# Performance work log

Hardware: AMD Instinct MI355X
Metric: run time of the kernel (lower is better)

## Reference

```python
import jax, jax.numpy as jnp
import numpy as np
from jax import lax

B, V, M, C, CM, D = 48, 16, 32, 48, 8, 128
VOCAB_V, VOCAB_M, OUT = 2000, 1000, 256


def setup_inputs() -> dict:
    key = jax.random.key(0)
    ks = jax.random.split(key, 22)
    s = 0.1  # keep GRU gates out of saturation
    return {
        "visit_ids": jax.random.randint(ks[0], (3, B, V, C), 0, VOCAB_V),
        "mon_ids": jax.random.randint(ks[1], (4, B, V, M, CM), 0, VOCAB_M),
        "weight_vals": jax.random.uniform(ks[2], (B, V)),
        "age_vals": jax.random.uniform(ks[3], (B, V)),
        "emb_visit": jax.random.normal(ks[4], (3, VOCAB_V, D)) * s,
        "emb_mon": jax.random.normal(ks[5], (4, VOCAB_M, D)) * s,
        "mgru_Wih": jax.random.normal(ks[6], (5, 3 * D, D)) * s,
        "mgru_Whh": jax.random.normal(ks[7], (5, 3 * D, D)) * s,
        "mgru_bih": jax.random.normal(ks[8], (5, 3 * D)) * s,
        "mgru_bhh": jax.random.normal(ks[9], (5, 3 * D)) * s,
        "vgru_Wih": jax.random.normal(ks[10], (7, 3 * D, D)) * s,
        "vgru_Whh": jax.random.normal(ks[11], (7, 3 * D, D)) * s,
        "vgru_bih": jax.random.normal(ks[12], (7, 3 * D)) * s,
        "vgru_bhh": jax.random.normal(ks[13], (7, 3 * D)) * s,
        "fc_weight_w": jax.random.normal(ks[14], (D, 1)) * s,
        "fc_weight_b": jax.random.normal(ks[15], (D,)) * s,
        "fc_age_w": jax.random.normal(ks[16], (D, 1)) * s,
        "fc_age_b": jax.random.normal(ks[17], (D,)) * s,
        "fc_out_w": jax.random.normal(ks[18], (OUT, 7 * D)) * s,
        "fc_out_b": jax.random.normal(ks[19], (OUT,)) * s,
    }


def gru_last(x, Wih, Whh, bih, bhh):
    """torch.nn.GRU(batch_first=True), return final hidden [N, D]."""
    xi = jnp.einsum('ntd,ed->nte', x, Wih) + bih  # [N, T, 3D] input projections
    h0 = jnp.zeros((x.shape[0], Whh.shape[1]), x.dtype)

    def step(h, gi):
        gh = h @ Whh.T + bhh
        ir, iz, inn = jnp.split(gi, 3, axis=-1)
        hr, hz, hn = jnp.split(gh, 3, axis=-1)
        r = jax.nn.sigmoid(ir + hr)
        z = jax.nn.sigmoid(iz + hz)
        n = jnp.tanh(inn + r * hn)
        return (1.0 - z) * n + z * h, None

    hT, _ = lax.scan(step, h0, jnp.swapaxes(xi, 0, 1))
    return hT


def reference(visit_ids, mon_ids, weight_vals, age_vals, emb_visit, emb_mon,
              mgru_Wih, mgru_Whh, mgru_bih, mgru_bhh,
              vgru_Wih, vgru_Whh, vgru_bih, vgru_bhh,
              fc_weight_w, fc_weight_b, fc_age_w, fc_age_b,
              fc_out_w, fc_out_b):
    # padding_idx=0 -> zero embedding row (dropout in eval mode = identity)
    ev = emb_visit.at[:, 0].set(0.0)
    em = emb_mon.at[:, 0].set(0.0)

    # visit-event embedding-bag: sum over code dim -> [B, V, D] per feature
    visit_origin = [jnp.sum(ev[k][visit_ids[k]], axis=2) for k in range(3)]

    def run_stream(t, mi, vi):
        # monitor-level GRU over M, then visit-level GRU over V
        h1 = gru_last(t, mgru_Wih[mi], mgru_Whh[mi], mgru_bih[mi], mgru_bhh[mi])
        h2 = gru_last(h1.reshape(B, V, D),
                      vgru_Wih[vi], vgru_Whh[vi], vgru_bih[vi], vgru_bhh[vi])
        return h2  # [B, D]

    # output slots in dict-insertion order: lab_item, cond, proc, drug, inj_item, weight, age
    slots = [None] * 7
    for p in range(2):  # (lab_item, lab_value), (inj_item, inj_value)
        # elementwise item*value embedding, summed over codes -> [B*V, M, D]
        mon = jnp.sum(em[2 * p][mon_ids[2 * p]] * em[2 * p + 1][mon_ids[2 * p + 1]],
                      axis=3).reshape(B * V, M, D)
        slots[0 if p == 0 else 4] = run_stream(mon, p, p)
        for k in range(3):  # visit features repeated along monitor dim
            t = jnp.broadcast_to(visit_origin[k][:, :, None, :],
                                 (B, V, M, D)).reshape(B * V, M, D)
            h = run_stream(t, 2 + k, 2 + k)
            slots[1 + k] = h if slots[1 + k] is None else slots[1 + k] + h

    # weight / age: Linear(1->D), zero-mask, visit-level GRU
    for vals, w, b, vi, slot in ((weight_vals, fc_weight_w, fc_weight_b, 5, 5),
                                 (age_vals, fc_age_w, fc_age_b, 6, 6)):
        xf = vals.reshape(-1, 1)
        h = (xf @ w.T + b) * (xf != 0)
        slots[slot] = gru_last(h.reshape(B, V, D),
                               vgru_Wih[vi], vgru_Whh[vi], vgru_bih[vi], vgru_bhh[vi])

    patient_emb = jnp.concatenate(slots, axis=-1)  # [B, 7D]
    return jax.nn.relu(patient_emb) @ fc_out_w.T + fc_out_b
```

## Files before the change

kernel.cpp:

```cpp
#include <hip/hip_runtime.h>
#include <stdint.h>


typedef unsigned short u16;
typedef uint32_t u32;
typedef short bf8 __attribute__((ext_vector_type(8)));
typedef float f4 __attribute__((ext_vector_type(4)));

static __device__ __forceinline__ float bf2f(u16 b){ u32 u=((u32)b)<<16; float f; __builtin_memcpy(&f,&u,4); return f; }
static __device__ __forceinline__ u16 f2bf(float f){ u32 u; __builtin_memcpy(&u,&f,4); u32 r=(u+0x7fffu+((u>>16)&1u))>>16; return (u16)r; }
static __device__ __forceinline__ float bflo(u32 u){ u32 x=u<<16; float f; __builtin_memcpy(&f,&x,4); return f; }
static __device__ __forceinline__ float bfhi(u32 u){ u32 x=u&0xffff0000u; float f; __builtin_memcpy(&f,&x,4); return f; }
static __device__ __forceinline__ f4 mfma16(bf8 a, bf8 b, f4 c){ return __builtin_amdgcn_mfma_f32_16x16x32_bf16(a,b,c,0,0,0); }

#if __has_builtin(__builtin_amdgcn_exp2f)
static __device__ __forceinline__ float fexp2(float x){ return __builtin_amdgcn_exp2f(x); }
#else
static __device__ __forceinline__ float fexp2(float x){ float r; asm volatile("v_exp_f32 %0, %1" : "=v"(r) : "v"(x)); return r; }
#endif
#if __has_builtin(__builtin_amdgcn_rcpf)
static __device__ __forceinline__ float frcp(float x){ return __builtin_amdgcn_rcpf(x); }
#else
static __device__ __forceinline__ float frcp(float x){ float r; asm volatile("v_rcp_f32 %0, %1" : "=v"(r) : "v"(x)); return r; }
#endif
#define LOG2E 1.44269504089f
static __device__ __forceinline__ float sigm(float x){ return frcp(1.0f + fexp2(-LOG2E*x)); }
static __device__ __forceinline__ float tanh_f(float x){ return 1.0f - 2.0f*frcp(1.0f + fexp2((2.0f*LOG2E)*x)); }

__global__ __launch_bounds__(256) void k_prep(
    const float* __restrict__ s0, const float* __restrict__ s1,
    const float* __restrict__ s2, const float* __restrict__ s3,
    const float* __restrict__ s4, const float* __restrict__ s5,
    u16* __restrict__ d0, u16* __restrict__ d1, u16* __restrict__ d2,
    u16* __restrict__ d3, u16* __restrict__ d4, u16* __restrict__ d5){
  int i = blockIdx.x*256 + threadIdx.x;
  const float* s; u16* d; int off;
  if      (i < 61440)  { s=s0; d=d0; off=i; }
  else if (i < 122880) { s=s1; d=d1; off=i-61440; }
  else if (i < 208896) { s=s2; d=d2; off=i-122880; }
  else if (i < 294912) { s=s3; d=d3; off=i-208896; }
  else if (i < 422912) { s=s4; d=d4; off=i-294912; }
  else if (i < 614912) { s=s5; d=d5; off=i-422912; }
  else return;
  float4 v = *(const float4*)(s + (size_t)off*4);
  ushort4 o = { f2bf(v.x), f2bf(v.y), f2bf(v.z), f2bf(v.w) };
  *(ushort4*)(d + (size_t)off*4) = o;
}

__global__ __launch_bounds__(256) void k_bags(const int* __restrict__ vids, const int* __restrict__ mids,
    const u16* __restrict__ embv_b, const u16* __restrict__ embm_b,
    const float* __restrict__ wv, const float* __restrict__ av,
    const float* __restrict__ ww, const float* __restrict__ wb,
    const float* __restrict__ aw, const float* __restrict__ ab,
    u16* __restrict__ mon_xT, u16* __restrict__ vis_org, u16* __restrict__ hin2T){
  int y = blockIdx.y;
  if (y < 2){
    int p = y;
    int rid = threadIdx.x >> 5, lane32 = threadIdx.x & 31, d0 = lane32*4;
    __shared__ int ids[8][16];
    if (threadIdx.x < 128){
      int rr = threadIdx.x >> 4, c = threadIdx.x & 15;
      int f = 2*p + (c>>3), cm = c & 7;
      ids[rr][c] = mids[((size_t)f*24576 + (size_t)blockIdx.x*8 + rr)*8 + cm];
    }
    __syncthreads();
    const u16* e1 = embm_b + (size_t)(2*p)*1000*128;
    const u16* e2 = embm_b + (size_t)(2*p+1)*1000*128;
    float a0=0.f,a1=0.f,a2=0.f,a3=0.f;
    #pragma unroll
    for (int c = 0; c < 8; ++c){
      int i1 = ids[rid][c], i2 = ids[rid][8+c];
      if (i1 && i2){
        uint2 a = *(const uint2*)(e1 + (size_t)i1*128 + d0);
        uint2 b = *(const uint2*)(e2 + (size_t)i2*128 + d0);
        a0 += bflo(a.x)*bflo(b.x); a1 += bfhi(a.x)*bfhi(b.x);
        a2 += bflo(a.y)*bflo(b.y); a3 += bfhi(a.y)*bfhi(b.y);
      }
    }
    size_t nm = (size_t)blockIdx.x*8 + rid;
    int bv = (int)(nm >> 5), m = (int)(nm & 31);
    ushort4 o = { f2bf(a0), f2bf(a1), f2bf(a2), f2bf(a3) };
    *(ushort4*)(mon_xT + (size_t)p*24576*128 + ((size_t)m*768 + bv)*128 + d0) = o;
  } else {
    int x = blockIdx.x;
    int sub = threadIdx.x >> 7, d = threadIdx.x & 127;
    if (x < 1152){
      __shared__ int ids[2][48];
      int row = x*2 + sub;
      int k = row / 768, bv = row - k*768;
      if (d < 48) ids[sub][d] = vids[((size_t)k*768 + bv)*48 + d];
      __syncthreads();
      const u16* eb = embv_b + (size_t)k*2000*128;
      float acc = 0.f;
      #pragma unroll 4
      for (int c = 0; c < 48; ++c){ int id = ids[sub][c]; if (id) acc += bf2f(eb[(size_t)id*128 + d]); }
      vis_org[((size_t)k*768 + bv)*128 + d] = f2bf(acc);
    } else if (x < 1920){
      int grow = (x - 1152)*2 + sub;
      int sidx = grow >= 768 ? 1 : 0;
      int row = grow - sidx*768;
      const float* vals = sidx ? av : wv;
      const float* wgt  = sidx ? aw : ww;
      const float* bias = sidx ? ab : wb;
      float v = vals[row];
      float h = (v != 0.f) ? (v * wgt[d] + bias[d]) : 0.f;
      int b = row >> 4, vv = row & 15;
      hin2T[((size_t)(5+sidx)*768 + (size_t)vv*48 + b)*128 + d] = f2bf(h);
    }
  }
}


#define BARRIER() asm volatile("s_waitcnt lgkmcnt(0)\n\ts_barrier" ::: "memory")

#define ALOAD(S, tt) { int t_=(tt); if (t_>=T) t_=0; \
  const u16* p_ = ap + (size_t)t_*rstride; \
  S[0]=*(const bf8*)(p_); S[1]=*(const bf8*)(p_+32); \
  S[2]=*(const bf8*)(p_+64); S[3]=*(const bf8*)(p_+96); }

#define GIMM(G0,G1,G2,S) { \
  f4 t0_={bs0_,bs0_,bs0_,bs0_}; G0=t0_; \
  f4 t1_={bs1_,bs1_,bs1_,bs1_}; G1=t1_; \
  f4 t2_={bin_,bin_,bin_,bin_}; G2=t2_; \
  G0=mfma16(S[0],wfi[0][0],G0); G0=mfma16(S[1],wfi[0][1],G0); \
  G0=mfma16(S[2],wfi[0][2],G0); G0=mfma16(S[3],wfi[0][3],G0); \
  G1=mfma16(S[0],wfi[1][0],G1); G1=mfma16(S[1],wfi[1][1],G1); \
  G1=mfma16(S[2],wfi[1][2],G1); G1=mfma16(S[3],wfi[1][3],G1); \
  G2=mfma16(S[0],wfi[2][0],G2); G2=mfma16(S[1],wfi[2][1],G2); \
  G2=mfma16(S[2],wfi[2][2],G2); G2=mfma16(S[3],wfi[2][3],G2); }

#define GH(G0,G1,AN) { \
  bf8 hf0_=*(const bf8*)&hlds[cur][lr][lq*8]; \
  bf8 hf1_=*(const bf8*)&hlds[cur][lr][32+lq*8]; \
  bf8 hf2_=*(const bf8*)&hlds[cur][lr][64+lq*8]; \
  bf8 hf3_=*(const bf8*)&hlds[cur][lr][96+lq*8]; \
  f4 an_={bhn_,bhn_,bhn_,bhn_}; AN=an_; \
  G0=mfma16(hf0_,wfh[0][0],G0); G0=mfma16(hf1_,wfh[0][1],G0); \
  G0=mfma16(hf2_,wfh[0][2],G0); G0=mfma16(hf3_,wfh[0][3],G0); \
  G1=mfma16(hf0_,wfh[1][0],G1); G1=mfma16(hf1_,wfh[1][1],G1); \
  G1=mfma16(hf2_,wfh[1][2],G1); G1=mfma16(hf3_,wfh[1][3],G1); \
  AN=mfma16(hf0_,wfh[2][0],AN); AN=mfma16(hf1_,wfh[2][1],AN); \
  AN=mfma16(hf2_,wfh[2][2],AN); AN=mfma16(hf3_,wfh[2][3],AN); }

#define GATES(G0,G1,G2,AN) { int nxt_=cur^1; \
  _Pragma("unroll") \
  for (int r=0;r<4;++r){ \
    float rr_=sigm(G0[r]); \
    float zz_=sigm(G1[r]); \
    float nn_=tanh_f(G2[r]+rr_*AN[r]); \
    float hv_=(1.0f-zz_)*nn_+zz_*hp[r]; hp[r]=hv_; \
    hlds[nxt_][lq*4+r][w*16+lr]=f2bf(hv_); } \
  BARRIER(); cur=nxt_; }

#define STEPB(G0,G1,G2,SN,tt) { \
  GH(G0,G1,ANr); \
  GATES(G0,G1,G2,ANr); \
  if ((tt)+2 < T){ GIMM(G0,G1,G2,SN); } \
  ALOAD(SN,(tt)+4); }

__global__ __launch_bounds__(512, 2) void k_gru(int phase,
    const u16* __restrict__ mon_xT, const u16* __restrict__ vis_org,
    u16* __restrict__ hin2T, u16* __restrict__ h2,
    const u16* __restrict__ mWih, const float* __restrict__ mbih,
    const u16* __restrict__ mWhh, const float* __restrict__ mbhh,
    const u16* __restrict__ vWih, const float* __restrict__ vbih,
    const u16* __restrict__ vWhh, const float* __restrict__ vbhh){
  int s = blockIdx.y, g = blockIdx.x;
  const u16* A; size_t rstride; int T, oMode; u16* ho;
  const u16 *Wi, *Wh; const float *biP, *bhP;
  if (phase == 0 && s < 5){
    T = 32; oMode = 0;
    if (s < 2){ A = mon_xT + (size_t)s*24576*128; rstride = 768*128; }
    else      { A = vis_org + (size_t)(s-2)*768*128; rstride = 0; }
    Wi = mWih + (size_t)s*49152; Wh = mWhh + (size_t)s*49152;
    biP = mbih + (size_t)s*384;  bhP = mbhh + (size_t)s*384;
    int slot = (0x32140u >> (4*s)) & 15;
    ho = hin2T + (size_t)slot*768*128;
  } else {
    if (g >= 3) return;
    T = 16; oMode = 1;
    A = hin2T + (size_t)s*768*128; rstride = 48*128;
    int vi = (0x6514320u >> (4*s)) & 15;
    Wi = vWih + (size_t)vi*49152; Wh = vWhh + (size_t)vi*49152;
    biP = vbih + (size_t)vi*384;  bhP = vbhh + (size_t)vi*384;
    ho = h2 + (size_t)s*48*128;
  }

  int w = threadIdx.x >> 6, l = threadIdx.x & 63;
  int lr = l & 15, lq = l >> 4;

  bf8 wfi[3][4], wfh[3][4];
  #pragma unroll
  for (int j = 0; j < 3; ++j){
    int colb = (w + 8*j)*16;
    const u16* wpi = Wi + (size_t)(colb + lr)*128 + lq*8;
    const u16* wph = Wh + (size_t)(colb + lr)*128 + lq*8;
    #pragma unroll
    for (int kt = 0; kt < 4; ++kt){
      wfi[j][kt] = *(const bf8*)(wpi + kt*32);
      wfh[j][kt] = *(const bf8*)(wph + kt*32);
    }
  }
  float bs0_ = biP[w*16 + lr]      + bhP[w*16 + lr];
  float bs1_ = biP[(8+w)*16 + lr]  + bhP[(8+w)*16 + lr];
  float bin_ = biP[(16+w)*16 + lr];
  float bhn_ = bhP[(16+w)*16 + lr];

  const u16* ap = A + (size_t)(g*16 + lr)*128 + lq*8;
  __shared__ u16 hlds[2][16][132];
  float hp[4] = {0.f,0.f,0.f,0.f};
  int cur = 0;
  f4 ANr;

  if (rstride){
    bf8 S0[4], S1[4];
    f4 gE0,gE1,gE2, gO0,gO1,gO2;
    ALOAD(S0,0); ALOAD(S1,1);
    GIMM(gE0,gE1,gE2,S0); ALOAD(S0,2);
    GIMM(gO0,gO1,gO2,S1); ALOAD(S1,3);
    {
      f4 an0={bhn_,bhn_,bhn_,bhn_}; ANr=an0;
      GATES(gE0,gE1,gE2,ANr);
    }
    GIMM(gE0,gE1,gE2,S0); ALOAD(S0,4);
    STEPB(gO0,gO1,gO2,S1,1);
    for (int t = 2; t < T; t += 2){
      STEPB(gE0,gE1,gE2,S0,t);
      STEPB(gO0,gO1,gO2,S1,t+1);
    }
  } else {
    f4 C0,C1,C2;
    {
      bf8 S0[4];
      ALOAD(S0,0);
      GIMM(C0,C1,C2,S0);
    }
    {
      f4 an0={bhn_,bhn_,bhn_,bhn_}; ANr=an0;
      GATES(C0,C1,C2,ANr);
    }
    for (int t = 1; t < T; ++t){
      f4 G0=C0, G1=C1;
      GH(G0,G1,ANr);
      GATES(G0,G1,C2,ANr);
    }
  }

  if (oMode == 0){
    #pragma unroll
    for (int r = 0; r < 4; ++r)
      ho[((size_t)(lq*4+r)*48 + g)*128 + w*16 + lr] = f2bf(hp[r]);
  } else {
    #pragma unroll
    for (int r = 0; r < 4; ++r)
      ho[((size_t)(g*16 + lq*4 + r))*128 + w*16 + lr] = f2bf(hp[r]);
  }
}

__global__ __launch_bounds__(256) void k_final(const u16* __restrict__ h2,
                                               const float* __restrict__ W,
                                               const float* __restrict__ Bias,
                                               float* __restrict__ out){
  int b = blockIdx.x, t = threadIdx.x;
  __shared__ float emb[896];
  for (int i = t; i < 896; i += 256){
    int j = i >> 7, d = i & 127;
    float v = bf2f(h2[((size_t)j*48 + b)*128 + d]);
    if (j >= 1 && j <= 3) v *= 2.0f;
    emb[i] = fmaxf(v, 0.f);
  }
  __syncthreads();
  float acc = Bias[t];
  const float* wp = W + (size_t)t*896;
  for (int i = 0; i < 896; i += 8){
    float4 w0 = *(const float4*)(wp + i);
    float4 w1 = *(const float4*)(wp + i + 4);
    acc += w0.x*emb[i]   + w0.y*emb[i+1] + w0.z*emb[i+2] + w0.w*emb[i+3];
    acc += w1.x*emb[i+4] + w1.y*emb[i+5] + w1.z*emb[i+6] + w1.w*emb[i+7];
  }
  out[(size_t)b*256 + t] = acc;
}

extern "C" void kernel_launch(void* const* d_in, const int* in_sizes, int n_in,
                              void* d_out, int out_size, void* d_ws, size_t ws_size,
                              hipStream_t stream){
  const int*   visit_ids   = (const int*)d_in[0];
  const int*   mon_ids     = (const int*)d_in[1];
  const float* weight_vals = (const float*)d_in[2];
  const float* age_vals    = (const float*)d_in[3];
  const float* emb_visit   = (const float*)d_in[4];
  const float* emb_mon     = (const float*)d_in[5];
  const float* mgru_Wih    = (const float*)d_in[6];
  const float* mgru_Whh    = (const float*)d_in[7];
  const float* mgru_bih    = (const float*)d_in[8];
  const float* mgru_bhh    = (const float*)d_in[9];
  const float* vgru_Wih    = (const float*)d_in[10];
  const float* vgru_Whh    = (const float*)d_in[11];
  const float* vgru_bih    = (const float*)d_in[12];
  const float* vgru_bhh    = (const float*)d_in[13];
  const float* fc_w_w      = (const float*)d_in[14];
  const float* fc_w_b      = (const float*)d_in[15];
  const float* fc_a_w      = (const float*)d_in[16];
  const float* fc_a_b      = (const float*)d_in[17];
  const float* fc_out_w    = (const float*)d_in[18];
  const float* fc_out_b    = (const float*)d_in[19];

  char* ws = (char*)d_ws;
  size_t o = 0;
  u16* mWih_b  = (u16*)(ws+o); o += 5ull*384*128*2;
  u16* mWhh_b  = (u16*)(ws+o); o += 5ull*384*128*2;
  u16* vWih_b  = (u16*)(ws+o); o += 7ull*384*128*2;
  u16* vWhh_b  = (u16*)(ws+o); o += 7ull*384*128*2;
  u16* embm_b  = (u16*)(ws+o); o += 4ull*1000*128*2;
  u16* embv_b  = (u16*)(ws+o); o += 3ull*2000*128*2;
  u16* mon_xT  = (u16*)(ws+o); o += 2ull*24576*128*2;
  u16* vis_org = (u16*)(ws+o); o += 3ull*768*128*2;
  u16* hin2T   = (u16*)(ws+o); o += 7ull*768*128*2;
  u16* h2      = (u16*)(ws+o); o += 7ull*48*128*2;

  k_prep<<<2402, 256, 0, stream>>>(mgru_Wih, mgru_Whh, vgru_Wih, vgru_Whh, emb_mon, emb_visit,
                                   mWih_b, mWhh_b, vWih_b, vWhh_b, embm_b, embv_b);
  k_bags<<<dim3(3072,3), 256, 0, stream>>>(visit_ids, mon_ids, embv_b, embm_b,
      weight_vals, age_vals, fc_w_w, fc_w_b, fc_a_w, fc_a_b,
      mon_xT, vis_org, hin2T);
  k_gru<<<dim3(48,7), 512, 0, stream>>>(0, mon_xT, vis_org, hin2T, h2,
      mWih_b, mgru_bih, mWhh_b, mgru_bhh, vWih_b, vgru_bih, vWhh_b, vgru_bhh);
  k_gru<<<dim3(3,5), 512, 0, stream>>>(1, mon_xT, vis_org, hin2T, h2,
      mWih_b, mgru_bih, mWhh_b, mgru_bhh, vWih_b, vgru_bih, vWhh_b, vgru_bhh);
  k_final<<<48, 256, 0, stream>>>(h2, fc_out_w, fc_out_b, (float*)d_out);
}
```

Before: 140.4 us.

## Fuse all stages into one cooperative persistent kernel with grid syncs

```diff
diff --git a/kernel.cpp b/kernel.cpp
--- a/kernel.cpp
+++ b/kernel.cpp
@@ -1,6 +1,9 @@
 #include <hip/hip_runtime.h>
+#include <hip/hip_cooperative_groups.h>
 #include <stdint.h>
 
+
+namespace cg = cooperative_groups;
 
 typedef unsigned short u16;
 typedef uint32_t u32;
@@ -24,94 +27,20 @@
 static __device__ __forceinline__ float frcp(float x){ float r; asm volatile("v_rcp_f32 %0, %1" : "=v"(r) : "v"(x)); return r; }
 #endif
 #define LOG2E 1.44269504089f
-static __device__ __forceinline__ float sigm(float x){ return frcp(1.0f + fexp2(-LOG2E*x)); }
-static __device__ __forceinline__ float tanh_f(float x){ return 1.0f - 2.0f*frcp(1.0f + fexp2((2.0f*LOG2E)*x)); }
-
-__global__ __launch_bounds__(256) void k_prep(
-    const float* __restrict__ s0, const float* __restrict__ s1,
-    const float* __restrict__ s2, const float* __restrict__ s3,
-    const float* __restrict__ s4, const float* __restrict__ s5,
-    u16* __restrict__ d0, u16* __restrict__ d1, u16* __restrict__ d2,
-    u16* __restrict__ d3, u16* __restrict__ d4, u16* __restrict__ d5){
-  int i = blockIdx.x*256 + threadIdx.x;
-  const float* s; u16* d; int off;
-  if      (i < 61440)  { s=s0; d=d0; off=i; }
-  else if (i < 122880) { s=s1; d=d1; off=i-61440; }
-  else if (i < 208896) { s=s2; d=d2; off=i-122880; }
-  else if (i < 294912) { s=s3; d=d3; off=i-208896; }
-  else if (i < 422912) { s=s4; d=d4; off=i-294912; }
-  else if (i < 614912) { s=s5; d=d5; off=i-422912; }
-  else return;
-  float4 v = *(const float4*)(s + (size_t)off*4);
-  ushort4 o = { f2bf(v.x), f2bf(v.y), f2bf(v.z), f2bf(v.w) };
-  *(ushort4*)(d + (size_t)off*4) = o;
-}
-
-__global__ __launch_bounds__(256) void k_bags(const int* __restrict__ vids, const int* __restrict__ mids,
-    const u16* __restrict__ embv_b, const u16* __restrict__ embm_b,
-    const float* __restrict__ wv, const float* __restrict__ av,
-    const float* __restrict__ ww, const float* __restrict__ wb,
-    const float* __restrict__ aw, const float* __restrict__ ab,
-    u16* __restrict__ mon_xT, u16* __restrict__ vis_org, u16* __restrict__ hin2T){
-  int y = blockIdx.y;
-  if (y < 2){
-    int p = y;
-    int rid = threadIdx.x >> 5, lane32 = threadIdx.x & 31, d0 = lane32*4;
-    __shared__ int ids[8][16];
-    if (threadIdx.x < 128){
-      int rr = threadIdx.x >> 4, c = threadIdx.x & 15;
-      int f = 2*p + (c>>3), cm = c & 7;
-      ids[rr][c] = mids[((size_t)f*24576 + (size_t)blockIdx.x*8 + rr)*8 + cm];
-    }
-    __syncthreads();
-    const u16* e1 = embm_b + (size_t)(2*p)*1000*128;
-    const u16* e2 = embm_b + (size_t)(2*p+1)*1000*128;
-    float a0=0.f,a1=0.f,a2=0.f,a3=0.f;
-    #pragma unroll
-    for (int c = 0; c < 8; ++c){
-      int i1 = ids[rid][c], i2 = ids[rid][8+c];
-      if (i1 && i2){
-        uint2 a = *(const uint2*)(e1 + (size_t)i1*128 + d0);
-        uint2 b = *(const uint2*)(e2 + (size_t)i2*128 + d0);
-        a0 += bflo(a.x)*bflo(b.x); a1 += bfhi(a.x)*bfhi(b.x);
-        a2 += bflo(a.y)*bflo(b.y); a3 += bfhi(a.y)*bfhi(b.y);
-      }
-    }
-    size_t nm = (size_t)blockIdx.x*8 + rid;
-    int bv = (int)(nm >> 5), m = (int)(nm & 31);
-    ushort4 o = { f2bf(a0), f2bf(a1), f2bf(a2), f2bf(a3) };
-    *(ushort4*)(mon_xT + (size_t)p*24576*128 + ((size_t)m*768 + bv)*128 + d0) = o;
-  } else {
-    int x = blockIdx.x;
-    int sub = threadIdx.x >> 7, d = threadIdx.x & 127;
-    if (x < 1152){
-      __shared__ int ids[2][48];
-      int row = x*2 + sub;
-      int k = row / 768, bv = row - k*768;
-      if (d < 48) ids[sub][d] = vids[((size_t)k*768 + bv)*48 + d];
-      __syncthreads();
-      const u16* eb = embv_b + (size_t)k*2000*128;
-      float acc = 0.f;
-      #pragma unroll 4
-      for (int c = 0; c < 48; ++c){ int id = ids[sub][c]; if (id) acc += bf2f(eb[(size_t)id*128 + d]); }
-      vis_org[((size_t)k*768 + bv)*128 + d] = f2bf(acc);
-    } else if (x < 1920){
-      int grow = (x - 1152)*2 + sub;
-      int sidx = grow >= 768 ? 1 : 0;
-      int row = grow - sidx*768;
-      const float* vals = sidx ? av : wv;
-      const float* wgt  = sidx ? aw : ww;
-      const float* bias = sidx ? ab : wb;
-      float v = vals[row];
-      float h = (v != 0.f) ? (v * wgt[d] + bias[d]) : 0.f;
-      int b = row >> 4, vv = row & 15;
-      hin2T[((size_t)(5+sidx)*768 + (size_t)vv*48 + b)*128 + d] = f2bf(h);
-    }
-  }
-}
-
+#define TWOL  2.88539008178f
+
+struct P {
+  const int *vids, *mids;
+  const float *embv, *embm, *wv, *av, *ww, *wb, *aw, *ab;
+  const float *mWih_f, *mWhh_f, *vWih_f, *vWhh_f;
+  const float *mbih, *mbhh, *vbih, *vbhh, *fcw, *fcb;
+  float* out;
+  u16 *mWih_b, *mWhh_b, *vWih_b, *vWhh_b, *embm_b, *embv_b;
+  u16 *mon_xT, *vis_org, *hin2T, *h2;
+};
 
 #define BARRIER() asm volatile("s_waitcnt lgkmcnt(0)\n\ts_barrier" ::: "memory")
+#define HL(b_,r_,c_) hl[(b_)*2112 + (r_)*132 + (c_)]
 
 #define ALOAD(S, tt) { int t_=(tt); if (t_>=T) t_=0; \
   const u16* p_ = ap + (size_t)t_*rstride; \
@@ -130,10 +59,10 @@
   G2=mfma16(S[2],wfi[2][2],G2); G2=mfma16(S[3],wfi[2][3],G2); }
 
 #define GH(G0,G1,AN) { \
-  bf8 hf0_=*(const bf8*)&hlds[cur][lr][lq*8]; \
-  bf8 hf1_=*(const bf8*)&hlds[cur][lr][32+lq*8]; \
-  bf8 hf2_=*(const bf8*)&hlds[cur][lr][64+lq*8]; \
-  bf8 hf3_=*(const bf8*)&hlds[cur][lr][96+lq*8]; \
+  bf8 hf0_=*(const bf8*)&HL(cur,lr,lq*8); \
+  bf8 hf1_=*(const bf8*)&HL(cur,lr,32+lq*8); \
+  bf8 hf2_=*(const bf8*)&HL(cur,lr,64+lq*8); \
+  bf8 hf3_=*(const bf8*)&HL(cur,lr,96+lq*8); \
   f4 an_={bhn_,bhn_,bhn_,bhn_}; AN=an_; \
   G0=mfma16(hf0_,wfh[0][0],G0); G0=mfma16(hf1_,wfh[0][1],G0); \
   G0=mfma16(hf2_,wfh[0][2],G0); G0=mfma16(hf3_,wfh[0][3],G0); \
@@ -145,11 +74,11 @@
 #define GATES(G0,G1,G2,AN) { int nxt_=cur^1; \
   _Pragma("unroll") \
   for (int r=0;r<4;++r){ \
-    float rr_=sigm(G0[r]); \
-    float zz_=sigm(G1[r]); \
-    float nn_=tanh_f(G2[r]+rr_*AN[r]); \
-    float hv_=(1.0f-zz_)*nn_+zz_*hp[r]; hp[r]=hv_; \
-    hlds[nxt_][lq*4+r][w*16+lr]=f2bf(hv_); } \
+    float rr_=frcp(1.0f+fexp2(G0[r])); \
+    float zz_=frcp(1.0f+fexp2(G1[r])); \
+    float nn_=1.0f-2.0f*frcp(1.0f+fexp2(G2[r]+rr_*AN[r])); \
+    float hv_=nn_+zz_*(hp[r]-nn_); hp[r]=hv_; \
+    HL(nxt_,lq*4+r,w*16+lr)=f2bf(hv_); } \
   BARRIER(); cur=nxt_; }
 
 #define STEPB(G0,G1,G2,SN,tt) { \
@@ -158,34 +87,25 @@
   if ((tt)+2 < T){ GIMM(G0,G1,G2,SN); } \
   ALOAD(SN,(tt)+4); }
 
-__global__ __launch_bounds__(512, 2) void k_gru(int phase,
-    const u16* __restrict__ mon_xT, const u16* __restrict__ vis_org,
-    u16* __restrict__ hin2T, u16* __restrict__ h2,
-    const u16* __restrict__ mWih, const float* __restrict__ mbih,
-    const u16* __restrict__ mWhh, const float* __restrict__ mbhh,
-    const u16* __restrict__ vWih, const float* __restrict__ vbih,
-    const u16* __restrict__ vWhh, const float* __restrict__ vbhh){
-  int s = blockIdx.y, g = blockIdx.x;
+static __device__ void gru_run(int mode, int s, int g, const P& p, u16* hl){
   const u16* A; size_t rstride; int T, oMode; u16* ho;
   const u16 *Wi, *Wh; const float *biP, *bhP;
-  if (phase == 0 && s < 5){
+  if (mode == 0){
     T = 32; oMode = 0;
-    if (s < 2){ A = mon_xT + (size_t)s*24576*128; rstride = 768*128; }
-    else      { A = vis_org + (size_t)(s-2)*768*128; rstride = 0; }
-    Wi = mWih + (size_t)s*49152; Wh = mWhh + (size_t)s*49152;
-    biP = mbih + (size_t)s*384;  bhP = mbhh + (size_t)s*384;
+    if (s < 2){ A = p.mon_xT + (size_t)s*24576*128; rstride = 768*128; }
+    else      { A = p.vis_org + (size_t)(s-2)*768*128; rstride = 0; }
+    Wi = p.mWih_b + (size_t)s*49152; Wh = p.mWhh_b + (size_t)s*49152;
+    biP = p.mbih + (size_t)s*384;  bhP = p.mbhh + (size_t)s*384;
     int slot = (0x32140u >> (4*s)) & 15;
-    ho = hin2T + (size_t)slot*768*128;
+    ho = p.hin2T + (size_t)slot*768*128;
   } else {
-    if (g >= 3) return;
     T = 16; oMode = 1;
-    A = hin2T + (size_t)s*768*128; rstride = 48*128;
+    A = p.hin2T + (size_t)s*768*128; rstride = 48*128;
     int vi = (0x6514320u >> (4*s)) & 15;
-    Wi = vWih + (size_t)vi*49152; Wh = vWhh + (size_t)vi*49152;
-    biP = vbih + (size_t)vi*384;  bhP = vbhh + (size_t)vi*384;
-    ho = h2 + (size_t)s*48*128;
-  }
-
+    Wi = p.vWih_b + (size_t)vi*49152; Wh = p.vWhh_b + (size_t)vi*49152;
+    biP = p.vbih + (size_t)vi*384;  bhP = p.vbhh + (size_t)vi*384;
+    ho = p.h2 + (size_t)s*48*128;
+  }
   int w = threadIdx.x >> 6, l = threadIdx.x & 63;
   int lr = l & 15, lq = l >> 4;
 
@@ -201,13 +121,12 @@
       wfh[j][kt] = *(const bf8*)(wph + kt*32);
     }
   }
-  float bs0_ = biP[w*16 + lr]      + bhP[w*16 + lr];
-  float bs1_ = biP[(8+w)*16 + lr]  + bhP[(8+w)*16 + lr];
-  float bin_ = biP[(16+w)*16 + lr];
-  float bhn_ = bhP[(16+w)*16 + lr];
+  float bs0_ = -LOG2E*(biP[w*16 + lr]     + bhP[w*16 + lr]);
+  float bs1_ = -LOG2E*(biP[(8+w)*16 + lr] + bhP[(8+w)*16 + lr]);
+  float bin_ =  TWOL*biP[(16+w)*16 + lr];
+  float bhn_ =  TWOL*bhP[(16+w)*16 + lr];
 
   const u16* ap = A + (size_t)(g*16 + lr)*128 + lq*8;
-  __shared__ u16 hlds[2][16][132];
   float hp[4] = {0.f,0.f,0.f,0.f};
   int cur = 0;
   f4 ANr;
@@ -218,10 +137,8 @@
     ALOAD(S0,0); ALOAD(S1,1);
     GIMM(gE0,gE1,gE2,S0); ALOAD(S0,2);
     GIMM(gO0,gO1,gO2,S1); ALOAD(S1,3);
-    {
-      f4 an0={bhn_,bhn_,bhn_,bhn_}; ANr=an0;
-      GATES(gE0,gE1,gE2,ANr);
-    }
+    { f4 an0={bhn_,bhn_,bhn_,bhn_}; ANr=an0;
+      GATES(gE0,gE1,gE2,ANr); }
     GIMM(gE0,gE1,gE2,S0); ALOAD(S0,4);
     STEPB(gO0,gO1,gO2,S1,1);
     for (int t = 2; t < T; t += 2){
@@ -230,15 +147,9 @@
     }
   } else {
     f4 C0,C1,C2;
-    {
-      bf8 S0[4];
-      ALOAD(S0,0);
-      GIMM(C0,C1,C2,S0);
-    }
-    {
-      f4 an0={bhn_,bhn_,bhn_,bhn_}; ANr=an0;
-      GATES(C0,C1,C2,ANr);
-    }
+    { bf8 S0[4]; ALOAD(S0,0); GIMM(C0,C1,C2,S0); }
+    { f4 an0={bhn_,bhn_,bhn_,bhn_}; ANr=an0;
+      GATES(C0,C1,C2,ANr); }
     for (int t = 1; t < T; ++t){
       f4 G0=C0, G1=C1;
       GH(G0,G1,ANr);
@@ -257,75 +168,172 @@
   }
 }
 
-__global__ __launch_bounds__(256) void k_final(const u16* __restrict__ h2,
-                                               const float* __restrict__ W,
-                                               const float* __restrict__ Bias,
-                                               float* __restrict__ out){
-  int b = blockIdx.x, t = threadIdx.x;
-  __shared__ float emb[896];
-  for (int i = t; i < 896; i += 256){
-    int j = i >> 7, d = i & 127;
-    float v = bf2f(h2[((size_t)j*48 + b)*128 + d]);
-    if (j >= 1 && j <= 3) v *= 2.0f;
-    emb[i] = fmaxf(v, 0.f);
-  }
-  __syncthreads();
-  float acc = Bias[t];
-  const float* wp = W + (size_t)t*896;
-  for (int i = 0; i < 896; i += 8){
-    float4 w0 = *(const float4*)(wp + i);
-    float4 w1 = *(const float4*)(wp + i + 4);
-    acc += w0.x*emb[i]   + w0.y*emb[i+1] + w0.z*emb[i+2] + w0.w*emb[i+3];
-    acc += w1.x*emb[i+4] + w1.y*emb[i+5] + w1.z*emb[i+6] + w1.w*emb[i+7];
-  }
-  out[(size_t)b*256 + t] = acc;
+__global__ __launch_bounds__(512, 2) void k_all(P p){
+  cg::grid_group grid = cg::this_grid();
+  int bid = blockIdx.x, tid = threadIdx.x;
+  __shared__ __align__(16) u16 hl[4224];
+  __shared__ int ids_s[256];
+  __shared__ float emb2[2][896];
+
+  {
+    int gi = bid*512 + tid;
+    for (int i = gi; i < 614912; i += 131072){
+      const float* s; u16* d; int off; bool scaled = false;
+      if      (i < 61440)  { s=p.mWih_f; d=p.mWih_b; off=i;        scaled=true; }
+      else if (i < 122880) { s=p.mWhh_f; d=p.mWhh_b; off=i-61440;  scaled=true; }
+      else if (i < 208896) { s=p.vWih_f; d=p.vWih_b; off=i-122880; scaled=true; }
+      else if (i < 294912) { s=p.vWhh_f; d=p.vWhh_b; off=i-208896; scaled=true; }
+      else if (i < 422912) { s=p.embm;   d=p.embm_b; off=i-294912; }
+      else                 { s=p.embv;   d=p.embv_b; off=i-422912; }
+      float sc = 1.0f;
+      if (scaled){ int row = (off >> 5) % 384; sc = (row < 256) ? -LOG2E : TWOL; }
+      float4 v = *(const float4*)(s + (size_t)off*4);
+      ushort4 o = { f2bf(v.x*sc), f2bf(v.y*sc), f2bf(v.z*sc), f2bf(v.w*sc) };
+      *(ushort4*)(d + (size_t)off*4) = o;
+    }
+  }
+  grid.sync();
+
+  {
+    for (int it = 0; it < 12; ++it){
+      int task = bid + it*256;
+      int pp = task / 1536, trow0 = (task - pp*1536) * 16;
+      if (tid < 256){
+        int rr = tid >> 4, c = tid & 15;
+        int f = 2*pp + (c >> 3), cm = c & 7;
+        ids_s[tid] = p.mids[((size_t)f*24576 + trow0 + rr)*8 + cm];
+      }
+      __syncthreads();
+      int rid = tid >> 5, lane = tid & 31, d0 = lane*4;
+      const u16* e1 = p.embm_b + (size_t)(2*pp)*128000;
+      const u16* e2 = p.embm_b + (size_t)(2*pp+1)*128000;
+      float a0=0.f,a1=0.f,a2=0.f,a3=0.f;
+      #pragma unroll
+      for (int c = 0; c < 8; ++c){
+        int i1 = ids_s[rid*16 + c], i2 = ids_s[rid*16 + 8 + c];
+        if (i1 && i2){
+          uint2 a = *(const uint2*)(e1 + (size_t)i1*128 + d0);
+          uint2 b = *(const uint2*)(e2 + (size_t)i2*128 + d0);
+          a0 += bflo(a.x)*bflo(b.x); a1 += bfhi(a.x)*bfhi(b.x);
+          a2 += bflo(a.y)*bflo(b.y); a3 += bfhi(a.y)*bfhi(b.y);
+        }
+      }
+      size_t nm = (size_t)trow0 + rid;
+      int bv = (int)(nm >> 5), m = (int)(nm & 31);
+      ushort4 o = { f2bf(a0), f2bf(a1), f2bf(a2), f2bf(a3) };
+      *(ushort4*)(p.mon_xT + (size_t)pp*24576*128 + ((size_t)m*768 + bv)*128 + d0) = o;
+      __syncthreads();
+    }
+    for (int it = 0; it < 3; ++it){
+      int task = bid + it*256;
+      bool act = task < 576;
+      if (act && tid < 192){
+        int rr = tid / 48, c = tid - rr*48;
+        int row = task*4 + rr;
+        int k = row / 768, bv = row - k*768;
+        ids_s[tid] = p.vids[((size_t)k*768 + bv)*48 + c];
+      }
+      __syncthreads();
+      if (act){
+        int sub = tid >> 7, d = tid & 127;
+        int row = task*4 + sub;
+        int k = row / 768, bv = row - k*768;
+        const u16* eb = p.embv_b + (size_t)k*256000;
+        float acc = 0.f;
+        #pragma unroll 4
+        for (int c = 0; c < 48; ++c){
+          int id = ids_s[sub*48 + c];
+          if (id) acc += bf2f(eb[(size_t)id*128 + d]);
+        }
+        p.vis_org[((size_t)k*768 + bv)*128 + d] = f2bf(acc);
+      }
+      __syncthreads();
+    }
+    for (int task = bid; task < 384; task += 256){
+      int sub = tid >> 7, d = tid & 127;
+      int grow = task*4 + sub;
+      int sidx = grow >= 768 ? 1 : 0;
+      int row = grow - sidx*768;
+      const float* vals = sidx ? p.av : p.wv;
+      const float* wgt  = sidx ? p.aw : p.ww;
+      const float* bias = sidx ? p.ab : p.wb;
+      float v = vals[row];
+      float h = (v != 0.f) ? (v * wgt[d] + bias[d]) : 0.f;
+      int b = row >> 4, vv = row & 15;
+      p.hin2T[((size_t)(5+sidx)*768 + (size_t)vv*48 + b)*128 + d] = f2bf(h);
+    }
+  }
+  grid.sync();
+
+  if (bid < 240) gru_run(0, bid/48, bid%48, p, hl);
+  grid.sync();
+
+  if (bid < 21) gru_run(1, bid/3, bid%3, p, hl);
+  grid.sync();
+
+  if (bid < 24){
+    int sub = tid >> 8, t = tid & 255;
+    int b = bid*2 + sub;
+    for (int i = t; i < 896; i += 256){
+      int j = i >> 7, d = i & 127;
+      float v = bf2f(p.h2[((size_t)j*48 + b)*128 + d]);
+      if (j >= 1 && j <= 3) v *= 2.0f;
+      emb2[sub][i] = fmaxf(v, 0.f);
+    }
+    __syncthreads();
+    float acc = p.fcb[t];
+    const float* wp = p.fcw + (size_t)t*896;
+    float* outp = p.out + (size_t)b*256 + t;
+    float s0 = 0.f;
+    for (int i = 0; i < 896; i += 8){
+      float4 w0 = *(const float4*)(wp + i);
+      float4 w1 = *(const float4*)(wp + i + 4);
+      s0 += w0.x*emb2[sub][i]   + w0.y*emb2[sub][i+1] + w0.z*emb2[sub][i+2] + w0.w*emb2[sub][i+3];
+      s0 += w1.x*emb2[sub][i+4] + w1.y*emb2[sub][i+5] + w1.z*emb2[sub][i+6] + w1.w*emb2[sub][i+7];
+    }
+    *outp = acc + s0;
+  }
 }
 
 extern "C" void kernel_launch(void* const* d_in, const int* in_sizes, int n_in,
                               void* d_out, int out_size, void* d_ws, size_t ws_size,
                               hipStream_t stream){
-  const int*   visit_ids   = (const int*)d_in[0];
-  const int*   mon_ids     = (const int*)d_in[1];
-  const float* weight_vals = (const float*)d_in[2];
-  const float* age_vals    = (const float*)d_in[3];
-  const float* emb_visit   = (const float*)d_in[4];
-  const float* emb_mon     = (const float*)d_in[5];
-  const float* mgru_Wih    = (const float*)d_in[6];
-  const float* mgru_Whh    = (const float*)d_in[7];
-  const float* mgru_bih    = (const float*)d_in[8];
-  const float* mgru_bhh    = (const float*)d_in[9];
-  const float* vgru_Wih    = (const float*)d_in[10];
-  const float* vgru_Whh    = (const float*)d_in[11];
-  const float* vgru_bih    = (const float*)d_in[12];
-  const float* vgru_bhh    = (const float*)d_in[13];
-  const float* fc_w_w      = (const float*)d_in[14];
-  const float* fc_w_b      = (const float*)d_in[15];
-  const float* fc_a_w      = (const float*)d_in[16];
-  const float* fc_a_b      = (const float*)d_in[17];
-  const float* fc_out_w    = (const float*)d_in[18];
-  const float* fc_out_b    = (const float*)d_in[19];
+  P prm;
+  prm.vids   = (const int*)d_in[0];
+  prm.mids   = (const int*)d_in[1];
+  prm.wv     = (const float*)d_in[2];
+  prm.av     = (const float*)d_in[3];
+  prm.embv   = (const float*)d_in[4];
+  prm.embm   = (const float*)d_in[5];
+  prm.mWih_f = (const float*)d_in[6];
+  prm.mWhh_f = (const float*)d_in[7];
+  prm.mbih   = (const float*)d_in[8];
+  prm.mbhh   = (const float*)d_in[9];
+  prm.vWih_f = (const float*)d_in[10];
+  prm.vWhh_f = (const float*)d_in[11];
+  prm.vbih   = (const float*)d_in[12];
+  prm.vbhh   = (const float*)d_in[13];
+  prm.ww     = (const float*)d_in[14];
+  prm.wb     = (const float*)d_in[15];
+  prm.aw     = (const float*)d_in[16];
+  prm.ab     = (const float*)d_in[17];
+  prm.fcw    = (const float*)d_in[18];
+  prm.fcb    = (const float*)d_in[19];
+  prm.out    = (float*)d_out;
 
   char* ws = (char*)d_ws;
   size_t o = 0;
-  u16* mWih_b  = (u16*)(ws+o); o += 5ull*384*128*2;
-  u16* mWhh_b  = (u16*)(ws+o); o += 5ull*384*128*2;
-  u16* vWih_b  = (u16*)(ws+o); o += 7ull*384*128*2;
-  u16* vWhh_b  = (u16*)(ws+o); o += 7ull*384*128*2;
-  u16* embm_b  = (u16*)(ws+o); o += 4ull*1000*128*2;
-  u16* embv_b  = (u16*)(ws+o); o += 3ull*2000*128*2;
-  u16* mon_xT  = (u16*)(ws+o); o += 2ull*24576*128*2;
-  u16* vis_org = (u16*)(ws+o); o += 3ull*768*128*2;
-  u16* hin2T   = (u16*)(ws+o); o += 7ull*768*128*2;
-  u16* h2      = (u16*)(ws+o); o += 7ull*48*128*2;
-
-  k_prep<<<2402, 256, 0, stream>>>(mgru_Wih, mgru_Whh, vgru_Wih, vgru_Whh, emb_mon, emb_visit,
-                                   mWih_b, mWhh_b, vWih_b, vWhh_b, embm_b, embv_b);
-  k_bags<<<dim3(3072,3), 256, 0, stream>>>(visit_ids, mon_ids, embv_b, embm_b,
-      weight_vals, age_vals, fc_w_w, fc_w_b, fc_a_w, fc_a_b,
-      mon_xT, vis_org, hin2T);
-  k_gru<<<dim3(48,7), 512, 0, stream>>>(0, mon_xT, vis_org, hin2T, h2,
-      mWih_b, mgru_bih, mWhh_b, mgru_bhh, vWih_b, vgru_bih, vWhh_b, vgru_bhh);
-  k_gru<<<dim3(3,5), 512, 0, stream>>>(1, mon_xT, vis_org, hin2T, h2,
-      mWih_b, mgru_bih, mWhh_b, mgru_bhh, vWih_b, vgru_bih, vWhh_b, vgru_bhh);
-  k_final<<<48, 256, 0, stream>>>(h2, fc_out_w, fc_out_b, (float*)d_out);
+  prm.mWih_b = (u16*)(ws+o); o += 5ull*384*128*2;
+  prm.mWhh_b = (u16*)(ws+o); o += 5ull*384*128*2;
+  prm.vWih_b = (u16*)(ws+o); o += 7ull*384*128*2;
+  prm.vWhh_b = (u16*)(ws+o); o += 7ull*384*128*2;
+  prm.embm_b = (u16*)(ws+o); o += 4ull*1000*128*2;
+  prm.embv_b = (u16*)(ws+o); o += 3ull*2000*128*2;
+  prm.mon_xT = (u16*)(ws+o); o += 2ull*24576*128*2;
+  prm.vis_org= (u16*)(ws+o); o += 3ull*768*128*2;
+  prm.hin2T  = (u16*)(ws+o); o += 7ull*768*128*2;
+  prm.h2     = (u16*)(ws+o); o += 7ull*48*128*2;
+
+  void* args[] = { &prm };
+  hipLaunchCooperativeKernel((void*)k_all, dim3(256), dim3(512), args, 0, stream);
 }
```

Result: slower. 321.6 us (+129.1%).
